# Kernel optimization log

Measured on AMD Instinct MI355X. Metric: run time of the kernel, lower is better.

Reference implementation:

```python
import jax, jax.numpy as jnp
import numpy as np

D_MODEL = 768
N_HEADS = 12
D_K = D_MODEL // N_HEADS


def setup_inputs() -> dict:
    key = jax.random.key(0)
    ks = jax.random.split(key, 11)
    B, T = 4, 2048
    s = 1.0 / np.sqrt(D_K)
    so = 1.0 / np.sqrt(D_MODEL)
    return {
        "q": jax.random.normal(ks[0], (B, T, D_MODEL), jnp.float32),
        "k": jax.random.normal(ks[1], (B, T, D_MODEL), jnp.float32),
        "v": jax.random.normal(ks[2], (B, T, D_MODEL), jnp.float32),
        "Wq": jax.random.normal(ks[3], (D_K, D_K), jnp.float32) * s,
        "bq": jax.random.normal(ks[4], (D_K,), jnp.float32) * s,
        "Wk": jax.random.normal(ks[5], (D_K, D_K), jnp.float32) * s,
        "bk": jax.random.normal(ks[6], (D_K,), jnp.float32) * s,
        "Wv": jax.random.normal(ks[7], (D_K, D_K), jnp.float32) * s,
        "bv": jax.random.normal(ks[8], (D_K,), jnp.float32) * s,
        "Wo": jax.random.normal(ks[9], (D_MODEL, D_MODEL), jnp.float32) * so,
        "bo": jax.random.normal(ks[10], (D_MODEL,), jnp.float32) * so,
    }


def reference(q, k, v, Wq, bq, Wk, bk, Wv, bv, Wo, bo):
    B, T, _ = q.shape
    # split into heads: [B, T, H, d_k]; per-head Linear shares weights across heads
    qh = q.reshape(B, T, N_HEADS, D_K)
    kh = k.reshape(B, T, N_HEADS, D_K)
    vh = v.reshape(B, T, N_HEADS, D_K)
    # torch Linear: x @ W^T + b, then transpose to [B, H, T, d_k]
    qh = jnp.einsum("bthd,ed->bhte", qh, Wq) + bq
    kh = jnp.einsum("bthd,ed->bhte", kh, Wk) + bk
    vh = jnp.einsum("bthd,ed->bhte", vh, Wv) + bv
    # scaled dot-product attention, full [B,H,T,T] scores (faithful to source)
    scores = jnp.einsum("bhqd,bhkd->bhqk", qh, kh) / jnp.sqrt(
        jnp.asarray(D_K, qh.dtype)
    )
    attn = jax.nn.softmax(scores, axis=-1)
    # einsum 'ijkl,ijlr->ikjr' -> output laid out [B, T, H, d_k]
    out_h = jnp.einsum("bhqk,bhkd->bqhd", attn, vh)
    concat = out_h.reshape(B, T, D_MODEL)
    return concat @ Wo.T + bo
```

## Files before the change

kernel.cpp:

```cpp
#include <hip/hip_runtime.h>


#define T_SEQ  2048
#define NH     12
#define DK     64
#define DMODEL 768
#define BATCH  4

typedef __attribute__((ext_vector_type(8))) short short8;
typedef __attribute__((ext_vector_type(4))) float f32x4;
typedef __attribute__((ext_vector_type(4))) unsigned short us4;

__device__ __forceinline__ float bf2f(unsigned short u) {
  union { unsigned int i; float f; } x; x.i = ((unsigned int)u) << 16; return x.f;
}
__device__ __forceinline__ unsigned short f2bf(float f) {
  union { float f; unsigned int i; } x; x.f = f;
  unsigned int r = x.i + 0x7fffu + ((x.i >> 16) & 1u);
  return (unsigned short)(r >> 16);
}
__device__ __forceinline__ us4 f4_to_bf4(float4 v) {
  us4 r; r.x = f2bf(v.x); r.y = f2bf(v.y); r.z = f2bf(v.z); r.w = f2bf(v.w); return r;
}


__global__ __launch_bounds__(256, 4)
void qkv_proj_kernel(const float* __restrict__ qin,
                     const float* __restrict__ kin,
                     const float* __restrict__ vin,
                     const float* __restrict__ Wq, const float* __restrict__ bq,
                     const float* __restrict__ Wk, const float* __restrict__ bk,
                     const float* __restrict__ Wv, const float* __restrict__ bv,
                     unsigned short* __restrict__ Qp,
                     unsigned short* __restrict__ Kp,
                     unsigned short* __restrict__ Vt)
{
  const int tt  = blockIdx.x;
  const int bh  = blockIdx.y;
  const int p   = blockIdx.z;
  const int b   = bh / NH, h = bh % NH;
  const int t0  = tt * 64;
  const int tid = threadIdx.x;
  const int wv  = tid >> 6;
  const int ln  = tid & 63;
  const int c   = ln & 15;
  const int qd  = ln >> 4;

  __shared__ __align__(16) unsigned short sX[64 * 72];
  __shared__ __align__(16) unsigned short sW[64 * 72];
  __shared__ __align__(16) unsigned short sVtr[64 * 68];

  const float* in = (p == 0) ? qin : (p == 1) ? kin : vin;
  const float* W  = (p == 0) ? Wq  : (p == 1) ? Wk  : Wv;
  const float* bs = (p == 0) ? bq  : (p == 1) ? bk  : bv;

  const int r0 = tid >> 4, g = tid & 15;
#pragma unroll
  for (int l = 0; l < 4; ++l) {
    int r = l * 16 + r0;
    float4 xv = *reinterpret_cast<const float4*>(in + ((size_t)(b * T_SEQ + t0 + r)) * DMODEL + h * DK + g * 4);
    *reinterpret_cast<us4*>(&sX[r * 72 + g * 4]) = f4_to_bf4(xv);
    float4 wvv = *reinterpret_cast<const float4*>(W + r * DK + g * 4);
    *reinterpret_cast<us4*>(&sW[r * 72 + g * 4]) = f4_to_bf4(wvv);
  }
  __syncthreads();

  short8 af[2];
#pragma unroll
  for (int kc = 0; kc < 2; ++kc)
    af[kc] = *reinterpret_cast<const short8*>(&sX[(wv * 16 + c) * 72 + kc * 32 + qd * 8]);

  f32x4 acc[4];
#pragma unroll
  for (int nb = 0; nb < 4; ++nb) {
    f32x4 a = {0.f, 0.f, 0.f, 0.f};
#pragma unroll
    for (int kc = 0; kc < 2; ++kc) {
      short8 bf = *reinterpret_cast<const short8*>(&sW[(nb * 16 + c) * 72 + kc * 32 + qd * 8]);
      a = __builtin_amdgcn_mfma_f32_16x16x32_bf16(af[kc], bf, a, 0, 0, 0);
    }
    acc[nb] = a;
  }

  if (p < 2) {
    unsigned short* outp = (p == 0) ? Qp : Kp;
#pragma unroll
    for (int nb = 0; nb < 4; ++nb) {
      int n = nb * 16 + c;
      float bias = bs[n];
#pragma unroll
      for (int r = 0; r < 4; ++r) {
        int t = t0 + wv * 16 + qd * 4 + r;
        outp[((size_t)bh * T_SEQ + t) * DK + n] = f2bf(acc[nb][r] + bias);
      }
    }
  } else {
#pragma unroll
    for (int nb = 0; nb < 4; ++nb) {
      int n = nb * 16 + c;
      float bias = bs[n];
#pragma unroll
      for (int r = 0; r < 4; ++r) {
        int row = wv * 16 + qd * 4 + r;
        sVtr[n * 68 + row] = f2bf(acc[nb][r] + bias);
      }
    }
    __syncthreads();
#pragma unroll
    for (int l = 0; l < 4; ++l) {
      int d = l * 16 + r0;
      us4 val = *reinterpret_cast<const us4*>(&sVtr[d * 68 + g * 4]);
      *reinterpret_cast<us4*>(Vt + ((size_t)bh * DK + d) * T_SEQ + t0 + g * 4) = val;
    }
  }
}

__global__ __launch_bounds__(256, 3)
void flash_kernel(const unsigned short* __restrict__ Qp,
                  const unsigned short* __restrict__ Kp,
                  const unsigned short* __restrict__ Vt,
                  unsigned short* __restrict__ concat)
{
  const int qt  = blockIdx.x;
  const int bh  = blockIdx.y;
  const int b   = bh / NH, h = bh % NH;
  const int tid = threadIdx.x;
  const int wv  = tid >> 6;
  const int ln  = tid & 63;
  const int c   = ln & 15;
  const int qd  = ln >> 4;

  __shared__ __align__(16) unsigned short sK[64 * 72];
  __shared__ __align__(16) unsigned short sV[64 * 72];
  __shared__ __align__(16) unsigned short sP[4][2][16 * 72];

  const int row0 = qt * 128 + wv * 32;

  short8 qf[2][2];
#pragma unroll
  for (int f = 0; f < 2; ++f) {
    const unsigned short* qb = Qp + ((size_t)bh * T_SEQ + row0 + f * 16 + c) * DK + qd * 8;
    qf[f][0] = *reinterpret_cast<const short8*>(qb);
    qf[f][1] = *reinterpret_cast<const short8*>(qb + 32);
  }

  const int r0 = tid >> 4, g = tid & 15;
  us4 kreg[4], vreg[4];
#define LOAD_TILE(J)                                                                   \
  {                                                                                    \
    _Pragma("unroll")                                                                  \
    for (int l = 0; l < 4; ++l) {                                                      \
      int r = l * 16 + r0;                                                             \
      kreg[l] = *reinterpret_cast<const us4*>(Kp + ((size_t)bh * T_SEQ + (J) * 64 + r) * DK + g * 4); \
      vreg[l] = *reinterpret_cast<const us4*>(Vt + ((size_t)bh * DK + r) * T_SEQ + (J) * 64 + g * 4); \
    }                                                                                  \
  }

  LOAD_TILE(0);

  f32x4 o[2][4];
  float lsum[2] = {0.f, 0.f};
#pragma unroll
  for (int f = 0; f < 2; ++f)
#pragma unroll
    for (int nb = 0; nb < 4; ++nb) o[f][nb] = (f32x4){0.f, 0.f, 0.f, 0.f};

  const float cexp = 0.125f * 1.44269504088896340736f;

  for (int j = 0; j < T_SEQ / 64; ++j) {
    __syncthreads();
#pragma unroll
    for (int l = 0; l < 4; ++l) {
      int r = l * 16 + r0;
      *reinterpret_cast<us4*>(&sK[r * 72 + g * 4]) = kreg[l];
      *reinterpret_cast<us4*>(&sV[r * 72 + g * 4]) = vreg[l];
    }
    __syncthreads();

    int jn = (j + 1) & (T_SEQ / 64 - 1);
    LOAD_TILE(jn);

    short8 kf[4][2];
#pragma unroll
    for (int nb = 0; nb < 4; ++nb) {
      kf[nb][0] = *reinterpret_cast<const short8*>(&sK[(nb * 16 + c) * 72 + qd * 8]);
      kf[nb][1] = *reinterpret_cast<const short8*>(&sK[(nb * 16 + c) * 72 + 32 + qd * 8]);
    }

    f32x4 st[2][4];
#pragma unroll
    for (int f = 0; f < 2; ++f)
#pragma unroll
      for (int nb = 0; nb < 4; ++nb) {
        f32x4 a = {0.f, 0.f, 0.f, 0.f};
        a = __builtin_amdgcn_mfma_f32_16x16x32_bf16(kf[nb][0], qf[f][0], a, 0, 0, 0);
        a = __builtin_amdgcn_mfma_f32_16x16x32_bf16(kf[nb][1], qf[f][1], a, 0, 0, 0);
        st[f][nb] = a;
      }

#pragma unroll
    for (int f = 0; f < 2; ++f) {
#pragma unroll
      for (int nb = 0; nb < 4; ++nb) {
        float p0 = __builtin_amdgcn_exp2f(st[f][nb][0] * cexp);
        float p1 = __builtin_amdgcn_exp2f(st[f][nb][1] * cexp);
        float p2 = __builtin_amdgcn_exp2f(st[f][nb][2] * cexp);
        float p3 = __builtin_amdgcn_exp2f(st[f][nb][3] * cexp);
        lsum[f] += (p0 + p1) + (p2 + p3);
        us4 pk; pk.x = f2bf(p0); pk.y = f2bf(p1); pk.z = f2bf(p2); pk.w = f2bf(p3);
        *reinterpret_cast<us4*>(&sP[wv][f][c * 72 + nb * 16 + qd * 4]) = pk;
      }
    }

    short8 pf[2][2];
#pragma unroll
    for (int f = 0; f < 2; ++f) {
      pf[f][0] = *reinterpret_cast<const short8*>(&sP[wv][f][c * 72 + qd * 8]);
      pf[f][1] = *reinterpret_cast<const short8*>(&sP[wv][f][c * 72 + 32 + qd * 8]);
    }

    short8 vf[4][2];
#pragma unroll
    for (int nb = 0; nb < 4; ++nb) {
      vf[nb][0] = *reinterpret_cast<const short8*>(&sV[(nb * 16 + c) * 72 + qd * 8]);
      vf[nb][1] = *reinterpret_cast<const short8*>(&sV[(nb * 16 + c) * 72 + 32 + qd * 8]);
    }

#pragma unroll
    for (int f = 0; f < 2; ++f)
#pragma unroll
      for (int nb = 0; nb < 4; ++nb) {
        o[f][nb] = __builtin_amdgcn_mfma_f32_16x16x32_bf16(pf[f][0], vf[nb][0], o[f][nb], 0, 0, 0);
        o[f][nb] = __builtin_amdgcn_mfma_f32_16x16x32_bf16(pf[f][1], vf[nb][1], o[f][nb], 0, 0, 0);
      }
  }

#pragma unroll
  for (int f = 0; f < 2; ++f) {
    lsum[f] += __shfl_xor(lsum[f], 16, 64);
    lsum[f] += __shfl_xor(lsum[f], 32, 64);
  }

#pragma unroll
  for (int f = 0; f < 2; ++f) {
#pragma unroll
    for (int r = 0; r < 4; ++r) {
      float lr = __shfl(lsum[f], qd * 4 + r, 16);
      int t = row0 + f * 16 + qd * 4 + r;
#pragma unroll
      for (int nb = 0; nb < 4; ++nb) {
        float val = o[f][nb][r] / lr;
        concat[((size_t)(b * T_SEQ + t)) * DMODEL + h * DK + nb * 16 + c] = f2bf(val);
      }
    }
  }
#undef LOAD_TILE
}

__global__ __launch_bounds__(256, 3)
void oproj_kernel(const unsigned short* __restrict__ A,
                  const float* __restrict__ Wo,
                  const float* __restrict__ bo,
                  float* __restrict__ out)
{
  const int nt  = blockIdx.x;
  const int mt  = blockIdx.y;
  const int tid = threadIdx.x;
  const int wv  = tid >> 6;
  const int ln  = tid & 63;
  const int c   = ln & 15;
  const int qd  = ln >> 4;

  __shared__ __align__(16) unsigned short sA[128 * 72];
  __shared__ __align__(16) unsigned short sB[64 * 72];

  const int r0 = tid >> 4, g = tid & 15;
  us4 areg[8];
  float4 breg[4];
#define LOAD_K(KK)                                                                       \
  {                                                                                      \
    _Pragma("unroll")                                                                    \
    for (int l = 0; l < 8; ++l)                                                          \
      areg[l] = *reinterpret_cast<const us4*>(A + ((size_t)(mt * 128 + l * 16 + r0)) * DMODEL + (KK) * 64 + g * 4); \
    _Pragma("unroll")                                                                    \
    for (int l = 0; l < 4; ++l)                                                          \
      breg[l] = *reinterpret_cast<const float4*>(Wo + ((size_t)(nt * 64 + l * 16 + r0)) * DMODEL + (KK) * 64 + g * 4); \
  }

  LOAD_K(0);

  f32x4 acc[2][4];
#pragma unroll
  for (int f = 0; f < 2; ++f)
#pragma unroll
    for (int nb = 0; nb < 4; ++nb) acc[f][nb] = (f32x4){0.f, 0.f, 0.f, 0.f};

  for (int kk = 0; kk < DMODEL / 64; ++kk) {
    __syncthreads();
#pragma unroll
    for (int l = 0; l < 8; ++l)
      *reinterpret_cast<us4*>(&sA[(l * 16 + r0) * 72 + g * 4]) = areg[l];
#pragma unroll
    for (int l = 0; l < 4; ++l)
      *reinterpret_cast<us4*>(&sB[(l * 16 + r0) * 72 + g * 4]) = f4_to_bf4(breg[l]);
    __syncthreads();

    int kn = kk + 1 < DMODEL / 64 ? kk + 1 : 0;
    LOAD_K(kn);

    short8 af[2][2];
#pragma unroll
    for (int f = 0; f < 2; ++f) {
      af[f][0] = *reinterpret_cast<const short8*>(&sA[(wv * 32 + f * 16 + c) * 72 + qd * 8]);
      af[f][1] = *reinterpret_cast<const short8*>(&sA[(wv * 32 + f * 16 + c) * 72 + 32 + qd * 8]);
    }
#pragma unroll
    for (int nb = 0; nb < 4; ++nb) {
      short8 b0 = *reinterpret_cast<const short8*>(&sB[(nb * 16 + c) * 72 + qd * 8]);
      short8 b1 = *reinterpret_cast<const short8*>(&sB[(nb * 16 + c) * 72 + 32 + qd * 8]);
#pragma unroll
      for (int f = 0; f < 2; ++f) {
        acc[f][nb] = __builtin_amdgcn_mfma_f32_16x16x32_bf16(af[f][0], b0, acc[f][nb], 0, 0, 0);
        acc[f][nb] = __builtin_amdgcn_mfma_f32_16x16x32_bf16(af[f][1], b1, acc[f][nb], 0, 0, 0);
      }
    }
  }

#pragma unroll
  for (int f = 0; f < 2; ++f)
#pragma unroll
    for (int nb = 0; nb < 4; ++nb) {
      int n = nt * 64 + nb * 16 + c;
      float bias = bo[n];
#pragma unroll
      for (int r = 0; r < 4; ++r) {
        int m = mt * 128 + wv * 32 + f * 16 + qd * 4 + r;
        out[(size_t)m * DMODEL + n] = acc[f][nb][r] + bias;
      }
    }
#undef LOAD_K
}

extern "C" void kernel_launch(void* const* d_in, const int* in_sizes, int n_in,
                              void* d_out, int out_size, void* d_ws, size_t ws_size,
                              hipStream_t stream) {
  const float* q  = (const float*)d_in[0];
  const float* k  = (const float*)d_in[1];
  const float* v  = (const float*)d_in[2];
  const float* Wq = (const float*)d_in[3];
  const float* bq = (const float*)d_in[4];
  const float* Wk = (const float*)d_in[5];
  const float* bk = (const float*)d_in[6];
  const float* Wv = (const float*)d_in[7];
  const float* bv = (const float*)d_in[8];
  const float* Wo = (const float*)d_in[9];
  const float* bo = (const float*)d_in[10];

  const size_t NTOK = (size_t)BATCH * T_SEQ;
  const size_t PER  = NTOK * DK * NH;
  unsigned short* Qp     = (unsigned short*)d_ws;
  unsigned short* Kp     = Qp + PER;
  unsigned short* Vt     = Kp + PER;
  unsigned short* concat = Vt + PER;

  dim3 blk(256);
  qkv_proj_kernel<<<dim3(32, BATCH * NH, 3), blk, 0, stream>>>(q, k, v, Wq, bq, Wk, bk, Wv, bv, Qp, Kp, Vt);
  flash_kernel<<<dim3(16, BATCH * NH), blk, 0, stream>>>(Qp, Kp, Vt, concat);
  oproj_kernel<<<dim3(12, 64), blk, 0, stream>>>(concat, Wo, bo, (float*)d_out);
}
```

Before: 234.1 us.

## Fold softmax scale into Q, use packed bf16 converts, widen oproj K-step

The softmax scale and log2e factor are folded into the Q projection, which removes a multiply per score in the flash loop. Probability conversion now uses the packed bf16x2 intrinsic, and the final normalisation uses a reciprocal-multiply instead of division. The flash kernel's launch bounds are raised to 4 waves per SIMD to increase occupancy, at the risk of register spills. The output-projection GEMM now uses a 128-wide K step with 16-byte loads, which halves the loop iterations and barriers but uses more LDS.

```diff
diff --git a/kernel.cpp b/kernel.cpp
--- a/kernel.cpp
+++ b/kernel.cpp
@@ -1,4 +1,5 @@
 #include <hip/hip_runtime.h>
+#include <hip/hip_bf16.h>
 
 
 #define T_SEQ  2048
@@ -10,10 +11,8 @@
 typedef __attribute__((ext_vector_type(8))) short short8;
 typedef __attribute__((ext_vector_type(4))) float f32x4;
 typedef __attribute__((ext_vector_type(4))) unsigned short us4;
-
-__device__ __forceinline__ float bf2f(unsigned short u) {
-  union { unsigned int i; float f; } x; x.i = ((unsigned int)u) << 16; return x.f;
-}
+typedef __attribute__((ext_vector_type(2))) unsigned int u32x2;
+
 __device__ __forceinline__ unsigned short f2bf(float f) {
   union { float f; unsigned int i; } x; x.f = f;
   unsigned int r = x.i + 0x7fffu + ((x.i >> 16) & 1u);
@@ -21,6 +20,11 @@
 }
 __device__ __forceinline__ us4 f4_to_bf4(float4 v) {
   us4 r; r.x = f2bf(v.x); r.y = f2bf(v.y); r.z = f2bf(v.z); r.w = f2bf(v.w); return r;
+}
+__device__ __forceinline__ unsigned int pack_bf2(float a, float b) {
+  union { __hip_bfloat162 h; unsigned int u; } x;
+  x.h = __float22bfloat162_rn(float2{a, b});
+  return x.u;
 }
 
 
@@ -82,8 +86,10 @@
     acc[nb] = a;
   }
 
+  const float cexp = 0.125f * 1.44269504088896340736f;
   if (p < 2) {
     unsigned short* outp = (p == 0) ? Qp : Kp;
+    const float mul = (p == 0) ? cexp : 1.0f;
 #pragma unroll
     for (int nb = 0; nb < 4; ++nb) {
       int n = nb * 16 + c;
@@ -91,7 +97,7 @@
 #pragma unroll
       for (int r = 0; r < 4; ++r) {
         int t = t0 + wv * 16 + qd * 4 + r;
-        outp[((size_t)bh * T_SEQ + t) * DK + n] = f2bf(acc[nb][r] + bias);
+        outp[((size_t)bh * T_SEQ + t) * DK + n] = f2bf((acc[nb][r] + bias) * mul);
       }
     }
   } else {
@@ -115,7 +121,7 @@
   }
 }
 
-__global__ __launch_bounds__(256, 3)
+__global__ __launch_bounds__(256, 4)
 void flash_kernel(const unsigned short* __restrict__ Qp,
                   const unsigned short* __restrict__ Kp,
                   const unsigned short* __restrict__ Vt,
@@ -165,8 +171,6 @@
 #pragma unroll
     for (int nb = 0; nb < 4; ++nb) o[f][nb] = (f32x4){0.f, 0.f, 0.f, 0.f};
 
-  const float cexp = 0.125f * 1.44269504088896340736f;
-
   for (int j = 0; j < T_SEQ / 64; ++j) {
     __syncthreads();
 #pragma unroll
@@ -202,13 +206,14 @@
     for (int f = 0; f < 2; ++f) {
 #pragma unroll
       for (int nb = 0; nb < 4; ++nb) {
-        float p0 = __builtin_amdgcn_exp2f(st[f][nb][0] * cexp);
-        float p1 = __builtin_amdgcn_exp2f(st[f][nb][1] * cexp);
-        float p2 = __builtin_amdgcn_exp2f(st[f][nb][2] * cexp);
-        float p3 = __builtin_amdgcn_exp2f(st[f][nb][3] * cexp);
+        float p0 = __builtin_amdgcn_exp2f(st[f][nb][0]);
+        float p1 = __builtin_amdgcn_exp2f(st[f][nb][1]);
+        float p2 = __builtin_amdgcn_exp2f(st[f][nb][2]);
+        float p3 = __builtin_amdgcn_exp2f(st[f][nb][3]);
         lsum[f] += (p0 + p1) + (p2 + p3);
-        us4 pk; pk.x = f2bf(p0); pk.y = f2bf(p1); pk.z = f2bf(p2); pk.w = f2bf(p3);
-        *reinterpret_cast<us4*>(&sP[wv][f][c * 72 + nb * 16 + qd * 4]) = pk;
+        u32x2 pku = {pack_bf2(p0, p1), pack_bf2(p2, p3)};
+        *reinterpret_cast<us4*>(&sP[wv][f][c * 72 + nb * 16 + qd * 4]) =
+            __builtin_bit_cast(us4, pku);
       }
     }
 
@@ -235,22 +240,23 @@
       }
   }
 
+  float linv[2];
 #pragma unroll
   for (int f = 0; f < 2; ++f) {
     lsum[f] += __shfl_xor(lsum[f], 16, 64);
     lsum[f] += __shfl_xor(lsum[f], 32, 64);
+    linv[f] = 1.0f / lsum[f];
   }
 
 #pragma unroll
   for (int f = 0; f < 2; ++f) {
 #pragma unroll
     for (int r = 0; r < 4; ++r) {
-      float lr = __shfl(lsum[f], qd * 4 + r, 16);
+      float lr = __shfl(linv[f], qd * 4 + r, 16);
       int t = row0 + f * 16 + qd * 4 + r;
 #pragma unroll
       for (int nb = 0; nb < 4; ++nb) {
-        float val = o[f][nb][r] / lr;
-        concat[((size_t)(b * T_SEQ + t)) * DMODEL + h * DK + nb * 16 + c] = f2bf(val);
+        concat[((size_t)(b * T_SEQ + t)) * DMODEL + h * DK + nb * 16 + c] = f2bf(o[f][nb][r] * lr);
       }
     }
   }
@@ -271,20 +277,23 @@
   const int c   = ln & 15;
   const int qd  = ln >> 4;
 
-  __shared__ __align__(16) unsigned short sA[128 * 72];
-  __shared__ __align__(16) unsigned short sB[64 * 72];
-
-  const int r0 = tid >> 4, g = tid & 15;
-  us4 areg[8];
-  float4 breg[4];
+  __shared__ __align__(16) unsigned short sA[128 * 136];
+  __shared__ __align__(16) unsigned short sB[64 * 136];
+
+  const int r16 = tid >> 4, g = tid & 15;
+  short8 areg[8];
+  float4 breg[4][2];
 #define LOAD_K(KK)                                                                       \
   {                                                                                      \
     _Pragma("unroll")                                                                    \
     for (int l = 0; l < 8; ++l)                                                          \
-      areg[l] = *reinterpret_cast<const us4*>(A + ((size_t)(mt * 128 + l * 16 + r0)) * DMODEL + (KK) * 64 + g * 4); \
+      areg[l] = *reinterpret_cast<const short8*>(A + ((size_t)(mt * 128 + l * 16 + r16)) * DMODEL + (KK) * 128 + g * 8); \
     _Pragma("unroll")                                                                    \
-    for (int l = 0; l < 4; ++l)                                                          \
-      breg[l] = *reinterpret_cast<const float4*>(Wo + ((size_t)(nt * 64 + l * 16 + r0)) * DMODEL + (KK) * 64 + g * 4); \
+    for (int l = 0; l < 4; ++l) {                                                        \
+      const float* wp = Wo + ((size_t)(nt * 64 + l * 16 + r16)) * DMODEL + (KK) * 128 + g * 8; \
+      breg[l][0] = *reinterpret_cast<const float4*>(wp);                                 \
+      breg[l][1] = *reinterpret_cast<const float4*>(wp + 4);                             \
+    }                                                                                    \
   }
 
   LOAD_K(0);
@@ -295,33 +304,30 @@
 #pragma unroll
     for (int nb = 0; nb < 4; ++nb) acc[f][nb] = (f32x4){0.f, 0.f, 0.f, 0.f};
 
-  for (int kk = 0; kk < DMODEL / 64; ++kk) {
+  for (int kk = 0; kk < DMODEL / 128; ++kk) {
     __syncthreads();
 #pragma unroll
     for (int l = 0; l < 8; ++l)
-      *reinterpret_cast<us4*>(&sA[(l * 16 + r0) * 72 + g * 4]) = areg[l];
-#pragma unroll
-    for (int l = 0; l < 4; ++l)
-      *reinterpret_cast<us4*>(&sB[(l * 16 + r0) * 72 + g * 4]) = f4_to_bf4(breg[l]);
-    __syncthreads();
-
-    int kn = kk + 1 < DMODEL / 64 ? kk + 1 : 0;
+      *reinterpret_cast<short8*>(&sA[(l * 16 + r16) * 136 + g * 8]) = areg[l];
+#pragma unroll
+    for (int l = 0; l < 4; ++l) {
+      *reinterpret_cast<us4*>(&sB[(l * 16 + r16) * 136 + g * 8]) = f4_to_bf4(breg[l][0]);
+      *reinterpret_cast<us4*>(&sB[(l * 16 + r16) * 136 + g * 8 + 4]) = f4_to_bf4(breg[l][1]);
+    }
+    __syncthreads();
+
+    int kn = kk + 1 < DMODEL / 128 ? kk + 1 : 0;
     LOAD_K(kn);
 
-    short8 af[2][2];
-#pragma unroll
-    for (int f = 0; f < 2; ++f) {
-      af[f][0] = *reinterpret_cast<const short8*>(&sA[(wv * 32 + f * 16 + c) * 72 + qd * 8]);
-      af[f][1] = *reinterpret_cast<const short8*>(&sA[(wv * 32 + f * 16 + c) * 72 + 32 + qd * 8]);
-    }
-#pragma unroll
-    for (int nb = 0; nb < 4; ++nb) {
-      short8 b0 = *reinterpret_cast<const short8*>(&sB[(nb * 16 + c) * 72 + qd * 8]);
-      short8 b1 = *reinterpret_cast<const short8*>(&sB[(nb * 16 + c) * 72 + 32 + qd * 8]);
-#pragma unroll
-      for (int f = 0; f < 2; ++f) {
-        acc[f][nb] = __builtin_amdgcn_mfma_f32_16x16x32_bf16(af[f][0], b0, acc[f][nb], 0, 0, 0);
-        acc[f][nb] = __builtin_amdgcn_mfma_f32_16x16x32_bf16(af[f][1], b1, acc[f][nb], 0, 0, 0);
+#pragma unroll
+    for (int kc = 0; kc < 4; ++kc) {
+      short8 af0 = *reinterpret_cast<const short8*>(&sA[(wv * 32 + c) * 136 + kc * 32 + qd * 8]);
+      short8 af1 = *reinterpret_cast<const short8*>(&sA[(wv * 32 + 16 + c) * 136 + kc * 32 + qd * 8]);
+#pragma unroll
+      for (int nb = 0; nb < 4; ++nb) {
+        short8 bfr = *reinterpret_cast<const short8*>(&sB[(nb * 16 + c) * 136 + kc * 32 + qd * 8]);
+        acc[0][nb] = __builtin_amdgcn_mfma_f32_16x16x32_bf16(af0, bfr, acc[0][nb], 0, 0, 0);
+        acc[1][nb] = __builtin_amdgcn_mfma_f32_16x16x32_bf16(af1, bfr, acc[1][nb], 0, 0, 0);
       }
     }
   }
```

Measured after the change: 247.2 us. 5.6% more time.
